# Kernel tuning notes

Measured on AMD Instinct MI355X. Metric: run time of the kernel, lower is better.

Reference implementation:

```python
import jax, jax.numpy as jnp
import numpy as np

B, L, P = 65536, 512, 96
E_LIN, E = 14, 16
FFT = 512
TEMP = 0.07
K = 2
EPS = 1e-5


def setup_inputs() -> dict:
    key = jax.random.key(0)
    k0, k1, k2 = jax.random.split(key, 3)
    x = jax.random.normal(k0, (B, L), dtype=jnp.float32)
    Wg = jax.random.normal(k1, (E, FFT // 2), dtype=jnp.float32) * 0.02
    bg = jnp.zeros((E,), dtype=jnp.float32)
    Wr = jax.random.normal(k2, (E_LIN, P, L), dtype=jnp.float32) * 0.02
    br = jnp.zeros((E_LIN, P), dtype=jnp.float32)
    return {"x": x, "Wg": Wg, "bg": bg, "Wr": Wr, "br": br}


def _periodogram(x):
    # x: [B, L] -> normalized power spectrum [B, FFT//2]
    x0 = x - jnp.mean(x, axis=1, keepdims=True)
    dft = jnp.fft.fft(x0, n=FFT, axis=1) / np.float32(np.sqrt(FFT))
    dft = dft[:, : FFT // 2]
    I = dft.real ** 2 + dft.imag ** 2
    s = jnp.sum(I, axis=1, keepdims=True)
    s = jnp.where(s == 0, jnp.ones_like(s), s)
    return I / s


def reference(x, Wg, bg, Wr, br):
    # gating (eval mode: no noise, divide by temperature)
    I = _periodogram(x)                                  # [B, F/2]
    gate = (I @ Wg.T + bg) / TEMP                        # [B, E]
    topv, topi = jax.lax.top_k(gate, K)                  # [B, K]
    gates = jax.nn.softmax(topv, axis=1)                 # [B, K]

    # RLinear experts: RevIN(norm) -> Linear -> RevIN(denorm); stats detached
    mu = jax.lax.stop_gradient(jnp.mean(x, axis=1, keepdims=True))        # [B,1]
    sd = jax.lax.stop_gradient(jnp.sqrt(jnp.var(x, axis=1, keepdims=True) + EPS))
    xn = (x - mu) / sd                                   # [B, L]
    yr = jnp.einsum('bl,epl->bep', xn, Wr) + br          # [B, E_LIN, P]
    yr = yr * sd[:, :, None] + mu[:, :, None]

    mean_out = jnp.broadcast_to(jnp.mean(x, axis=1, keepdims=True), (x.shape[0], P))[:, None, :]
    naive_out = jnp.broadcast_to(x[:, -1:], (x.shape[0], P))[:, None, :]

    eo = jnp.concatenate([yr, mean_out, naive_out], axis=1)   # [B, E, P]
    sel = jnp.take_along_axis(eo, topi[:, :, None], axis=1)   # [B, K, P]
    out = jnp.sum(gates[:, :, None] * sel, axis=1)            # [B, P]
    return out
```

## Files before the change

### kernel.cpp

```cpp
#include <hip/hip_runtime.h>
#include <math.h>

#define NB_B 65536
#define NL   512
#define NP   96
#define NE   16
#define NEL  14
#define NF   256
#define TEMP_INV (1.0f/0.07f)
#define TAU  1e-5f
#define PI_D 3.14159265358979323846
#define MAXCHK 1536

typedef __attribute__((ext_vector_type(8))) short bf16x8;
typedef __attribute__((ext_vector_type(4))) float f32x4;


#define WS_PCNT     0
#define WS_HOLES    16384
#define WS_PBASE    32768
#define WS_FLAGCNT  33792
#define WS_NCHK     33824
#define WS_HOLECNT  33840
#define WS_FLAG     33856
#define WS_SSUM     296000
#define WS_WGT      301376
#define WS_BGT      317760
#define WS_TWD      319872
#define WS_REC      328064
#define WS_HDR      590208
#define WS_RIDX     1638784
#define WS_WRB      1900928
#define WS_DESC     3473792
#define WS_XB16     3480064

__device__ __forceinline__ unsigned short f2bf(float f) {
    unsigned u = __float_as_uint(f);
    unsigned r = (u + 0x7fffu + ((u >> 16) & 1u)) >> 16;
    return (unsigned short)r;
}

__global__ __launch_bounds__(256) void k_prep(
    const float* __restrict__ Wg, const float* __restrict__ bg,
    const float* __restrict__ Wr,
    float* __restrict__ Ssum, float* __restrict__ WgE, float* __restrict__ bgT,
    double2* __restrict__ twd,
    int* __restrict__ pcnt, int* __restrict__ flagcnt, int* __restrict__ holecnt,
    ushort4* __restrict__ Wrb, int perm)
{
    int g = blockIdx.x * 256 + threadIdx.x;
    {
        ushort4 o = make_ushort4(0, 0, 0, 0);
        if (g < NEL * NP * NL / 4) {
            float4 v;
            if (perm) {
                int row = g >> 7, sq = g & 127;
                int ll = sq >> 1, kb = (sq & 1) * 4;
                const float* wr = Wr + (size_t)row * NL + ll;
                v.x = wr[(kb + 0) * 64]; v.y = wr[(kb + 1) * 64];
                v.z = wr[(kb + 2) * 64]; v.w = wr[(kb + 3) * 64];
            } else {
                v = ((const float4*)Wr)[g];
            }
            o.x = f2bf(v.x); o.y = f2bf(v.y); o.z = f2bf(v.z); o.w = f2bf(v.w);
        }
        Wrb[g] = o;
    }
    if (g < NEL * NP * 8) {
        int row = g >> 3, seg = g & 7;
        const float4* w = (const float4*)(Wr + (size_t)row * NL + seg * 64);
        float s = 0.f;
#pragma unroll
        for (int i = 0; i < 16; i++) { float4 v = w[i]; s += v.x + v.y + v.z + v.w; }
        s += __shfl_xor(s, 1); s += __shfl_xor(s, 2); s += __shfl_xor(s, 4);
        if (seg == 0) Ssum[row] = s;
    }
    if (g < 4096) {
        int c = g & 3, e = (g >> 2) & 15, f4 = g >> 6;
        WgE[g] = Wg[e * NF + f4 * 4 + c] * TEMP_INV;
    }
    if (g < 512) {
        double a = -2.0 * PI_D * (double)g / 512.0;
        twd[g] = make_double2(cos(a), sin(a));
    }
    if (g < 256) pcnt[g << 4] = 0;
    if (g < NE) bgT[g] = bg[g] * TEMP_INV;
    if (g == 300) *flagcnt = 0;
    if (g == 301) *holecnt = 0;
}

__global__ __launch_bounds__(256) void k_gate(
    const float* __restrict__ x,
    const float4* __restrict__ WgE4, const float* __restrict__ bgT,
    int* __restrict__ rec, float4* __restrict__ hdr,
    int* __restrict__ flaglist, int* __restrict__ flagcnt,
    int* __restrict__ pcnt, unsigned short* __restrict__ xb16)
{
    __shared__ __align__(16) float2 s_z[4][576];
    float* s_Iv = (float*)&s_z[0][0];

    const int t = threadIdx.x;
    const int wv = t >> 6, l = t & 63;
    const int b0 = blockIdx.x * 8 + wv * 2;

    const float th = -6.283185307179586f / 512.0f;
    const float R2 = 0.70710678118654752f;
    float s1, c1; __sincosf((float)l * th, &s1, &c1);
    float s2, c2; __sincosf((float)(2 * l) * th, &s2, &c2);
    float sw0, cw0; __sincosf((float)((l & 31) << 3) * th, &sw0, &cw0);
    float sw1, cw1; __sincosf((float)((l & 15) << 4) * th, &sw1, &cw1);
    float sw2, cw2; __sincosf((float)((l & 7) << 5) * th, &sw2, &cw2);
    float2 tw0[4];
    tw0[0] = make_float2(c1, s1);
    tw0[1] = make_float2(R2 * (c1 + s1), R2 * (s1 - c1));
    tw0[2] = make_float2(s1, -c1);
    tw0[3] = make_float2(tw0[1].y, -tw0[1].x);
    float2 tw1[2];
    tw1[0] = make_float2(c2, s2);
    tw1[1] = make_float2(s2, -c2);
    const float2 w2 = make_float2(c2 * c2 - s2 * s2, 2.f * c2 * s2);
    float2 wst[5];
    wst[0] = make_float2(cw0, sw0);
    wst[1] = make_float2(cw1, sw1);
    wst[2] = make_float2(cw2, sw2);
    {
        int j2 = l & 3;
        float cc3 = (j2 == 0) ? 1.f : (j2 == 1) ? R2 : (j2 == 2) ? 0.f : -R2;
        float ss3 = (j2 == 0) ? 0.f : (j2 == 2) ? -1.f : -R2;
        wst[3] = make_float2(cc3, ss3);
    }
    wst[4] = (l & 1) ? make_float2(0.f, -1.f) : make_float2(1.f, 0.f);

    const float* xa = x + (size_t)b0 * NL;
    const float* xb = xa + NL;
    float xr[8], xi[8];
#pragma unroll
    for (int k = 0; k < 8; k++) { xr[k] = xa[k * 64 + l]; xi[k] = xb[k * 64 + l]; }
    const float last_a = __shfl(xr[7], 63);
    const float last_b = __shfl(xi[7], 63);

    if (xb16) {
        unsigned pa_[4], pb_[4];
#pragma unroll
        for (int j = 0; j < 4; j++) {
            asm("v_cvt_pk_bf16_f32 %0, %1, %2" : "=v"(pa_[j]) : "v"(xr[2 * j]), "v"(xr[2 * j + 1]));
            asm("v_cvt_pk_bf16_f32 %0, %1, %2" : "=v"(pb_[j]) : "v"(xi[2 * j]), "v"(xi[2 * j + 1]));
        }
        *(uint4*)(xb16 + (size_t)b0 * NL + l * 8)       = *(uint4*)pa_;
        *(uint4*)(xb16 + (size_t)(b0 + 1) * NL + l * 8) = *(uint4*)pb_;
    }

#pragma unroll
    for (int k = 0; k < 4; k++) {
        float2 w = tw0[k];
        float ur = xr[k], ui = xi[k], vr = xr[k + 4], vi = xi[k + 4];
        xr[k] = ur + vr; xi[k] = ui + vi;
        float dr = ur - vr, di = ui - vi;
        xr[k + 4] = dr * w.x - di * w.y; xi[k + 4] = dr * w.y + di * w.x;
    }
    {
        const int kk[4] = {0, 1, 4, 5};
#pragma unroll
        for (int g2 = 0; g2 < 4; g2++) {
            int k = kk[g2];
            float2 w = tw1[k & 1];
            float ur = xr[k], ui = xi[k], vr = xr[k + 2], vi = xi[k + 2];
            xr[k] = ur + vr; xi[k] = ui + vi;
            float dr = ur - vr, di = ui - vi;
            xr[k + 2] = dr * w.x - di * w.y; xi[k + 2] = dr * w.y + di * w.x;
        }
    }
    {
#pragma unroll
        for (int k = 0; k < 8; k += 2) {
            float ur = xr[k], ui = xi[k], vr = xr[k + 1], vi = xi[k + 1];
            xr[k] = ur + vr; xi[k] = ui + vi;
            float dr = ur - vr, di = ui - vi;
            xr[k + 1] = dr * w2.x - di * w2.y; xi[k + 1] = dr * w2.y + di * w2.x;
        }
    }
#pragma unroll
    for (int st = 3; st < 8; st++) {
        const int half = 256 >> st;
        const float2 w = wst[st - 3];
        const bool up = (l & half) != 0;
        const float sg = up ? -1.f : 1.f;
        const float cc = up ? w.x : 1.f;
        const float ss = up ? w.y : 0.f;
#pragma unroll
        for (int k = 0; k < 8; k++) {
            float pr = __shfl_xor(xr[k], half);
            float pi = __shfl_xor(xi[k], half);
            float tr = fmaf(sg, xr[k], pr);
            float ti = fmaf(sg, xi[k], pi);
            xr[k] = tr * cc - ti * ss;
            xi[k] = tr * ss + ti * cc;
        }
    }
    {
        const float sg = (l & 1) ? -1.f : 1.f;
#pragma unroll
        for (int k = 0; k < 8; k++) {
            float pr = __shfl_xor(xr[k], 1);
            float pi = __shfl_xor(xi[k], 1);
            xr[k] = fmaf(sg, xr[k], pr);
            xi[k] = fmaf(sg, xi[k], pi);
        }
    }

#pragma unroll
    for (int k = 0; k < 8; k++) {
        int i = k * 64 + l;
        s_z[wv][i + (i >> 3)] = make_float2(xr[k], xi[k]);
    }

    float Ia[4], Ib[4];
    float psa = 0.f, psb = 0.f;
#pragma unroll
    for (int j = 0; j < 4; j++) {
        int f = (l << 2) | j;
        int i1_ = (int)(__brev((unsigned)f) >> 23);
        int i2_ = (int)(__brev((unsigned)((512 - f) & 511)) >> 23);
        float2 z1 = s_z[wv][i1_ + (i1_ >> 3)];
        float2 z2 = s_z[wv][i2_ + (i2_ >> 3)];
        float pr_ = z1.x + z2.x, qm = z1.y - z2.y;
        float qp = z1.y + z2.y, pm = z1.x - z2.x;
        float va = pr_ * pr_ + qm * qm;
        float vb = qp * qp + pm * pm;
        if (f == 0) { va = 0.f; vb = 0.f; }
        Ia[j] = va; Ib[j] = vb;
        psa += va; psb += vb;
    }
#pragma unroll
    for (int m = 1; m < 64; m <<= 1) {
        psa += __shfl_xor(psa, m); psb += __shfl_xor(psb, m);
    }
    const float psa_raw = psa, psb_raw = psb;
    if (psa == 0.f) psa = 1.f;
    if (psb == 0.f) psb = 1.f;
    const float inv_a = 1.f / psa, inv_b = 1.f / psb;

    const float2 Z0   = s_z[wv][0];
    const float2 Z256 = s_z[wv][1];

    float* wI = s_Iv + wv * 1152;
    const int io = (l << 2) + ((l >> 4) << 2);
    *(float4*)(wI + io)       = make_float4(Ia[0], Ia[1], Ia[2], Ia[3]);
    *(float4*)(wI + 272 + io) = make_float4(Ib[0], Ib[1], Ib[2], Ib[3]);

    const int e16 = l & 15, cq = l >> 4;
    const float bgv = bgT[e16];
    float accA = 0.f, accB = 0.f;
    const float* rA = wI + cq * 68;
    const float* rB = rA + 272;
#pragma unroll 4
    for (int jj = 0; jj < 16; jj++) {
        float4 ia = *(const float4*)(rA + 4 * jj);
        float4 ib = *(const float4*)(rB + 4 * jj);
        float4 w = WgE4[(cq * 16 + jj) * 16 + e16];
        accA += ia.x * w.x + ia.y * w.y + ia.z * w.z + ia.w * w.w;
        accB += ib.x * w.x + ib.y * w.y + ib.z * w.z + ib.w * w.w;
    }
    accA += __shfl_xor(accA, 16); accA += __shfl_xor(accA, 32);
    accB += __shfl_xor(accB, 16); accB += __shfl_xor(accB, 32);

    float v = ((l & 16) ? accB * inv_b : accA * inv_a) + bgv;

    float b0v = v; int b0i = e16;
#pragma unroll
    for (int m = 1; m < 16; m <<= 1) {
        float ov = __shfl_xor(b0v, m); int oi = __shfl_xor(b0i, m);
        if (ov > b0v || (ov == b0v && oi < b0i)) { b0v = ov; b0i = oi; }
    }
    float v1 = (e16 == b0i) ? -1e30f : v;
    float b1v = v1; int b1i = e16;
#pragma unroll
    for (int m = 1; m < 16; m <<= 1) {
        float ov = __shfl_xor(b1v, m); int oi = __shfl_xor(b1i, m);
        if (ov > b1v || (ov == b1v && oi < b1i)) { b1v = ov; b1i = oi; }
    }
    float v2 = (e16 == b1i) ? -1e30f : v1;
    float b2v = v2;
#pragma unroll
    for (int m = 1; m < 16; m <<= 1) {
        float ov = __shfl_xor(b2v, m);
        b2v = fmaxf(b2v, ov);
    }

    if (l == 0 || l == 16) {
        const int r = l >> 4;
        const int b = b0 + r;
        const float mu = (r ? Z0.y : Z0.x) * (1.f / 512.f);
        const float Jv = r ? Z256.y : Z256.x;
        const float ps = r ? psb_raw : psa_raw;
        const float sd = sqrtf((0.5f * ps + Jv * Jv) * (1.f / 262144.f) + 1e-5f);
        const float last = r ? last_b : last_a;
        const float w0 = 1.f / (1.f + expf(b1v - b0v));
        const int pid = b0i * 16 + b1i;
        const int lo = atomicAdd(&pcnt[pid << 4], 1);
        rec[b] = (pid << 24) | lo;
        hdr[b] = make_float4(mu, sd, last, w0);
        if (b1v - b2v < TAU) {
            int pos = atomicAdd(flagcnt, 1);
            flaglist[pos] = b;
        }
    }
}

__global__ __launch_bounds__(256) void k_refine(
    const float* __restrict__ x, const double2* __restrict__ twd,
    const float* __restrict__ Wg, const float* __restrict__ bg,
    int* __restrict__ rec, float4* __restrict__ hdr,
    const int* __restrict__ flaglist, const int* __restrict__ flagcnt,
    int* __restrict__ pcnt, int* __restrict__ holes, int* __restrict__ holecnt)
{
    __shared__ double s_x[512];
    __shared__ double s_I[256];
    __shared__ double s_red[16];
    __shared__ double s_g[16];
    const int nf = *flagcnt;
    const int t = threadIdx.x;
    const int wid = t >> 6, lane = t & 63;
    for (int fi = blockIdx.x; fi < nf; fi += gridDim.x) {
        const int b = flaglist[fi];
        const float* xp = x + (size_t)b * NL;
        double v0 = (double)xp[t], v1 = (double)xp[t + 256];
        double lsum = v0 + v1;
        for (int m = 1; m < 64; m <<= 1) lsum += __shfl_xor(lsum, m);
        if (lane == 0) s_red[wid] = lsum;
        __syncthreads();
        double mu = (s_red[0] + s_red[1] + s_red[2] + s_red[3]) * (1.0 / 512.0);
        s_x[t] = v0 - mu; s_x[t + 256] = v1 - mu;
        __syncthreads();
        double2 w = twd[t];
        double pr = 1.0, pi = 0.0, cr = 0.0, ci = 0.0;
        for (int n = 0; n < 512; n++) {
            double xv = s_x[n];
            cr += xv * pr; ci += xv * pi;
            double t2 = pr * w.x - pi * w.y;
            pi = pr * w.y + pi * w.x;
            pr = t2;
        }
        double I = cr * cr + ci * ci;
        s_I[t] = I;
        double ls = I;
        for (int m = 1; m < 64; m <<= 1) ls += __shfl_xor(ls, m);
        if (lane == 0) s_red[8 + wid] = ls;
        __syncthreads();
        double stot = s_red[8] + s_red[9] + s_red[10] + s_red[11];
        if (stot == 0.0) stot = 1.0;
        if (t < 16) {
            double acc = 0.0;
            const float* wrow = Wg + t * NF;
            for (int f = 0; f < NF; f++) acc += s_I[f] * (double)wrow[f];
            s_g[t] = (acc / stot + (double)bg[t]) * (1.0 / 0.07);
        }
        __syncthreads();
        if (t == 0) {
            double c0 = -1e300, c1 = -1e300; int j0 = 0, j1 = 0;
            for (int i = 0; i < 16; i++) {
                double v = s_g[i];
                if (v > c0) { c1 = c0; j1 = j0; c0 = v; j0 = i; }
                else if (v > c1) { c1 = v; j1 = i; }
            }
            double e1 = exp(c1 - c0);
            float w0f = (float)(1.0 / (1.0 + e1));
            int newpid = j0 * 16 + j1;
            int oldrec = rec[b];
            int oldpid = (int)(((unsigned)oldrec) >> 24);
            if (newpid == oldpid) {
                ((float*)(hdr + b))[3] = w0f;
            } else {
                int pos = atomicAdd(holecnt, 1);
                if (pos < 4096) {
                    int nlo = atomicAdd(&pcnt[newpid << 4], 1);
                    rec[b] = (newpid << 24) | nlo;
                    holes[pos] = oldrec;
                    ((float*)(hdr + b))[3] = w0f;
                }
            }
        }
        __syncthreads();
    }
}

__global__ __launch_bounds__(256) void k_scan(
    const int* __restrict__ pcnt, int* __restrict__ pbase,
    int* __restrict__ desc, int* __restrict__ nchk)
{
    __shared__ int s[256], c[256];
    const int t = threadIdx.x;
    const int n = pcnt[t << 4];
    s[t] = n;
    c[t] = (n + 63) >> 6;
    __syncthreads();
    for (int off = 1; off < 256; off <<= 1) {
        int v1 = (t >= off) ? s[t - off] : 0;
        int v2 = (t >= off) ? c[t - off] : 0;
        __syncthreads();
        s[t] += v1; c[t] += v2;
        __syncthreads();
    }
    int excl = t ? s[t - 1] : 0;
    int cexcl = t ? c[t - 1] : 0;
    pbase[t] = excl;
    int myc = (n + 63) >> 6;
    for (int j = 0; j < myc; j++) desc[cexcl + j] = (t << 16) | j;
    if (t == 255) *nchk = cexcl + myc;
}

__global__ __launch_bounds__(256) void k_scatter(
    const int* __restrict__ rec, const int* __restrict__ pbase,
    int* __restrict__ ridx,
    const int* __restrict__ holes, const int* __restrict__ holecnt)
{
    const int t = threadIdx.x;
    const int b = blockIdx.x * 256 + t;
    unsigned v = (unsigned)rec[b];
    ridx[pbase[v >> 24] + (v & 0xFFFFFF)] = b;
    if (blockIdx.x == 0) {
        int nh = *holecnt; if (nh > 4096) nh = 4096;
        for (int h = t; h < nh; h += 256) {
            unsigned hv = (unsigned)holes[h];
            ridx[pbase[hv >> 24] + (hv & 0xFFFFFF)] = -1;
        }
    }
}

template<int XB>
__global__ __launch_bounds__(256) void k_gemm(
    const float* __restrict__ x, const unsigned short* __restrict__ xb16,
    const unsigned short* __restrict__ Wrb,
    const float* __restrict__ br, const float* __restrict__ Ssum,
    const float4* __restrict__ hdr, float* __restrict__ out,
    const int* __restrict__ pcnt, const int* __restrict__ pbase,
    const int* __restrict__ ridx,
    const int* __restrict__ desc, const int* __restrict__ nchk)
{
    __shared__ __align__(16) unsigned short sA[64 * 72];
    __shared__ __align__(16) unsigned short sB[2][96 * 72];
    __shared__ int    s_idx[64];
    __shared__ float4 s_hdr[64];
    __shared__ float  s_br[2][96], s_S[2][96];
    if ((int)blockIdx.x >= *nchk) return;
    const int d = desc[blockIdx.x];
    const int pid = d >> 16, cc = d & 0xffff;
    const int n = pcnt[pid << 4];
    const int base = pbase[pid];
    const int i0 = pid >> 4, i1 = pid & 15;
    const int t = threadIdx.x;
    const int lane = t & 63, wv = t >> 6;
    const int quad = lane >> 4, l16 = lane & 15;
    const int ar = t >> 2, asub = t & 3;
    if (t < 96) {
        s_br[0][t] = (i0 < NEL) ? br[i0 * NP + t] : 0.f;
        s_S [0][t] = (i0 < NEL) ? Ssum[i0 * NP + t] : 0.f;
        s_br[1][t] = (i1 < NEL) ? br[i1 * NP + t] : 0.f;
        s_S [1][t] = (i1 < NEL) ? Ssum[i1 * NP + t] : 0.f;
    }
    if (t < 64) {
        int g = cc * 64 + t;
        bool vld = g < n;
        int row = vld ? ridx[base + g] : -1;
        s_idx[t] = row;
        s_hdr[t] = (row >= 0) ? hdr[row] : make_float4(0.f, 0.f, 0.f, 0.f);
    }
    __syncthreads();

    f32x4 acc[2][6];
#pragma unroll
    for (int ex = 0; ex < 2; ex++)
#pragma unroll
        for (int j = 0; j < 6; j++) acc[ex][j] = (f32x4){0.f, 0.f, 0.f, 0.f};

    int rr = s_idx[ar]; if (rr < 0) rr = 0;

    unsigned boff[6];
    unsigned short* bdst[6];
    const unsigned short* wb[2];
    wb[0] = Wrb + (size_t)i0 * NP * NL;
    wb[1] = Wrb + (size_t)i1 * NP * NL;
    int bex[6];
#pragma unroll
    for (int it = 0; it < 6; it++) {
        int ex = (it >= 3);
        int fl = t + (it - 3 * ex) * 256;
        int p = fl >> 3, kg = fl & 7;
        bex[it] = ex;
        boff[it] = (unsigned)(p * NL + kg * 8);
        bdst[it] = &sB[ex][p * 72 + kg * 8];
    }
    unsigned short* adst = sA + ar * 72 + asub * 16;

    const unsigned short* xrow16 = xb16 + (size_t)rr * NL + asub * 16;
    const float* xrowf = x + (size_t)rr * NL + asub * 16;

    bf16x8 aR[2]; float4 fA[4]; bf16x8 bR[6];

    if constexpr (XB) {
        aR[0] = *(const bf16x8*)(xrow16);
        aR[1] = *(const bf16x8*)(xrow16 + 8);
    } else {
#pragma unroll
        for (int i = 0; i < 4; i++) fA[i] = ((const float4*)xrowf)[i];
    }
#pragma unroll
    for (int it = 0; it < 6; it++) bR[it] = *(const bf16x8*)(wb[bex[it]] + boff[it]);

    for (int kb = 0; kb < NL; kb += 64) {
        if constexpr (XB) {
            *(bf16x8*)adst       = aR[0];
            *(bf16x8*)(adst + 8) = aR[1];
        } else {
            unsigned short tmp[16];
#pragma unroll
            for (int i = 0; i < 4; i++) {
                float4 v = fA[i];
                tmp[i * 4 + 0] = f2bf(v.x); tmp[i * 4 + 1] = f2bf(v.y);
                tmp[i * 4 + 2] = f2bf(v.z); tmp[i * 4 + 3] = f2bf(v.w);
            }
            *(bf16x8*)adst       = *(bf16x8*)tmp;
            *(bf16x8*)(adst + 8) = *(bf16x8*)(tmp + 8);
        }
#pragma unroll
        for (int it = 0; it < 6; it++) *(bf16x8*)bdst[it] = bR[it];
        __syncthreads();

        const int kn = kb + 64;
        if (kn < NL) {
            if constexpr (XB) {
                aR[0] = *(const bf16x8*)(xrow16 + kn);
                aR[1] = *(const bf16x8*)(xrow16 + kn + 8);
            } else {
#pragma unroll
                for (int i = 0; i < 4; i++) fA[i] = ((const float4*)(xrowf + kn))[i];
            }
#pragma unroll
            for (int it = 0; it < 6; it++)
                bR[it] = *(const bf16x8*)(wb[bex[it]] + boff[it] + kn);
        }

#pragma unroll
        for (int ks = 0; ks < 2; ks++) {
            bf16x8 af = *(const bf16x8*)(sA + (wv * 16 + l16) * 72 + ks * 32 + quad * 8);
#pragma unroll
            for (int ex = 0; ex < 2; ex++)
#pragma unroll
                for (int nt = 0; nt < 6; nt++) {
                    bf16x8 bf = *(const bf16x8*)(&sB[ex][(nt * 16 + l16) * 72 + ks * 32 + quad * 8]);
                    acc[ex][nt] = __builtin_amdgcn_mfma_f32_16x16x32_bf16(af, bf, acc[ex][nt], 0, 0, 0);
                }
        }
        __syncthreads();
    }
#pragma unroll
    for (int i = 0; i < 4; i++) {
        int rloc = wv * 16 + quad * 4 + i;
        int row = s_idx[rloc];
        if (row >= 0) {
            float4 h = s_hdr[rloc];
            float mu = h.x, sd = h.y, last = h.z, w0 = h.w, w1 = 1.f - w0;
            float* orow = out + (size_t)row * NP;
#pragma unroll
            for (int nt = 0; nt < 6; nt++) {
                int p = nt * 16 + l16;
                float v0 = (i0 < NEL) ? (mu + s_br[0][p] * sd - mu * s_S[0][p] + acc[0][nt][i])
                                      : (i0 == NEL ? mu : last);
                float v1 = (i1 < NEL) ? (mu + s_br[1][p] * sd - mu * s_S[1][p] + acc[1][nt][i])
                                      : (i1 == NEL ? mu : last);
                orow[p] = w0 * v0 + w1 * v1;
            }
        }
    }
}

extern "C" void kernel_launch(void* const* d_in, const int* in_sizes, int n_in,
                              void* d_out, int out_size, void* d_ws, size_t ws_size,
                              hipStream_t stream)
{
    const float* x  = (const float*)d_in[0];
    const float* Wg = (const float*)d_in[1];
    const float* bg = (const float*)d_in[2];
    const float* Wr = (const float*)d_in[3];
    const float* br = (const float*)d_in[4];
    float* out = (float*)d_out;
    char* ws = (char*)d_ws;

    int*     pcnt     = (int*)(ws + WS_PCNT);
    int*     holes    = (int*)(ws + WS_HOLES);
    int*     pbase    = (int*)(ws + WS_PBASE);
    int*     flagcnt  = (int*)(ws + WS_FLAGCNT);
    int*     nchk     = (int*)(ws + WS_NCHK);
    int*     holecnt  = (int*)(ws + WS_HOLECNT);
    int*     flaglist = (int*)(ws + WS_FLAG);
    float*   Ssum     = (float*)(ws + WS_SSUM);
    float*   WgE      = (float*)(ws + WS_WGT);
    float*   bgT      = (float*)(ws + WS_BGT);
    double2* twd      = (double2*)(ws + WS_TWD);
    int*     rec      = (int*)(ws + WS_REC);
    float4*  hdr      = (float4*)(ws + WS_HDR);
    int*     ridx     = (int*)(ws + WS_RIDX);
    unsigned short* Wrb = (unsigned short*)(ws + WS_WRB);
    int*     desc     = (int*)(ws + WS_DESC);

    const size_t xb_bytes = (size_t)NB_B * NL * 2;
    const int use_xb = (ws_size >= (size_t)WS_XB16 + xb_bytes);
    unsigned short* xb16 = use_xb ? (unsigned short*)(ws + WS_XB16) : (unsigned short*)0;

    k_prep<<<dim3(768), dim3(256), 0, stream>>>(Wg, bg, Wr, Ssum, WgE, bgT, twd,
                                                pcnt, flagcnt, holecnt,
                                                (ushort4*)Wrb, use_xb);
    k_gate<<<dim3(NB_B / 8), dim3(256), 0, stream>>>(x, (const float4*)WgE, bgT,
                                                     rec, hdr, flaglist, flagcnt, pcnt, xb16);
    k_refine<<<dim3(512), dim3(256), 0, stream>>>(x, twd, Wg, bg, rec, hdr,
                                                  flaglist, flagcnt, pcnt, holes, holecnt);
    k_scan<<<dim3(1), dim3(256), 0, stream>>>(pcnt, pbase, desc, nchk);
    k_scatter<<<dim3(NB_B / 256), dim3(256), 0, stream>>>(rec, pbase, ridx, holes, holecnt);
    if (use_xb)
        k_gemm<1><<<dim3(MAXCHK), dim3(256), 0, stream>>>(x, xb16, Wrb, br, Ssum, hdr, out,
                                                          pcnt, pbase, ridx, desc, nchk);
    else
        k_gemm<0><<<dim3(MAXCHK), dim3(256), 0, stream>>>(x, xb16, Wrb, br, Ssum, hdr, out,
                                                          pcnt, pbase, ridx, desc, nchk);
}
```

Baseline: 296.7 us.

## Add register-direct MFMA GEMM with pre-swizzled bf16 expert weight fragments

Adds a second bf16 copy of the expert weights, pre-arranged in k_prep into the exact MFMA B-fragment order so each lane loads its operand with one contiguous 16-byte read. A new GEMM kernel reads A fragments from the bf16 copy of x and B fragments straight from global memory into registers, dropping the shared-memory staging and barriers of the old tiled kernel. Each block computes both selected experts for 64 rows and applies the RevIN denorm and gate blend in the epilogue. The cost is heavy register use, about 24 bf16x8 B fragments in flight per k-step, and repeated weight reads served from cache instead of LDS. The new path also needs a larger workspace and falls back to the old kernel when the workspace is too small.

```diff
diff --git a/kernel.cpp b/kernel.cpp
--- a/kernel.cpp
+++ b/kernel.cpp
@@ -33,6 +33,8 @@
 #define WS_WRB      1900928
 #define WS_DESC     3473792
 #define WS_XB16     3480064
+#define WS_WRBF     70588928
+#define WS_WRBF_END 72161792
 
 __device__ __forceinline__ unsigned short f2bf(float f) {
     unsigned u = __float_as_uint(f);
@@ -46,7 +48,7 @@
     float* __restrict__ Ssum, float* __restrict__ WgE, float* __restrict__ bgT,
     double2* __restrict__ twd,
     int* __restrict__ pcnt, int* __restrict__ flagcnt, int* __restrict__ holecnt,
-    ushort4* __restrict__ Wrb, int perm)
+    ushort4* __restrict__ Wrb, ushort4* __restrict__ WrbF, int perm)
 {
     int g = blockIdx.x * 256 + threadIdx.x;
     {
@@ -65,6 +67,33 @@
             o.x = f2bf(v.x); o.y = f2bf(v.y); o.z = f2bf(v.z); o.w = f2bf(v.w);
         }
         Wrb[g] = o;
+    }
+    if (WrbF) {
+        ushort4 o = make_ushort4(0, 0, 0, 0);
+        int idx  = g >> 1;
+        int lane = idx & 63;
+        int idx2 = idx >> 6;
+        int nt   = idx2 % 6;
+        int idx3 = idx2 / 6;
+        int ks   = idx3 & 1;
+        int idx4 = idx3 >> 1;
+        int kb8  = idx4 & 7;
+        int e    = idx4 >> 3;
+        if (e < NEL) {
+            int p = nt * 16 + (lane & 15);
+            int quad = lane >> 4;
+            int skb = kb8 * 64 + ks * 32 + quad * 8 + (g & 1) * 4;
+            const float* wr = Wr + ((size_t)e * NP + p) * NL;
+            float vv[4];
+#pragma unroll
+            for (int jj = 0; jj < 4; jj++) {
+                int sk = skb + jj;
+                int ko = perm ? ((sk & 7) * 64 + (sk >> 3)) : sk;
+                vv[jj] = wr[ko];
+            }
+            o.x = f2bf(vv[0]); o.y = f2bf(vv[1]); o.z = f2bf(vv[2]); o.w = f2bf(vv[3]);
+        }
+        WrbF[g] = o;
     }
     if (g < NEL * NP * 8) {
         int row = g >> 3, seg = g & 7;
@@ -423,6 +452,97 @@
         for (int h = t; h < nh; h += 256) {
             unsigned hv = (unsigned)holes[h];
             ridx[pbase[hv >> 24] + (hv & 0xFFFFFF)] = -1;
+        }
+    }
+}
+
+__global__ __launch_bounds__(256) void k_gemm_reg(
+    const unsigned short* __restrict__ xb16,
+    const unsigned short* __restrict__ WrbF,
+    const float* __restrict__ br, const float* __restrict__ Ssum,
+    const float4* __restrict__ hdr, float* __restrict__ out,
+    const int* __restrict__ pcnt, const int* __restrict__ pbase,
+    const int* __restrict__ ridx,
+    const int* __restrict__ desc, const int* __restrict__ nchk)
+{
+    __shared__ int    s_idx[64];
+    __shared__ float4 s_hdr[64];
+    __shared__ float  s_br[2][96], s_S[2][96];
+    if ((int)blockIdx.x >= *nchk) return;
+    const int d = desc[blockIdx.x];
+    const int pid = d >> 16, cc = d & 0xffff;
+    const int n = pcnt[pid << 4];
+    const int base = pbase[pid];
+    const int i0 = pid >> 4, i1 = pid & 15;
+    const int t = threadIdx.x;
+    const int lane = t & 63, wv = t >> 6;
+    const int quad = lane >> 4, l16 = lane & 15;
+    if (t < 96) {
+        s_br[0][t] = (i0 < NEL) ? br[i0 * NP + t] : 0.f;
+        s_S [0][t] = (i0 < NEL) ? Ssum[i0 * NP + t] : 0.f;
+        s_br[1][t] = (i1 < NEL) ? br[i1 * NP + t] : 0.f;
+        s_S [1][t] = (i1 < NEL) ? Ssum[i1 * NP + t] : 0.f;
+    }
+    if (t < 64) {
+        int g = cc * 64 + t;
+        bool vld = g < n;
+        int row = vld ? ridx[base + g] : -1;
+        s_idx[t] = row;
+        s_hdr[t] = (row >= 0) ? hdr[row] : make_float4(0.f, 0.f, 0.f, 0.f);
+    }
+    __syncthreads();
+
+    int myrow = s_idx[wv * 16 + l16]; if (myrow < 0) myrow = 0;
+    const unsigned short* aP = xb16 + (size_t)myrow * NL + quad * 8;
+    const unsigned short* bP[2];
+    bP[0] = WrbF + (size_t)i0 * 49152 + lane * 8;
+    bP[1] = WrbF + (size_t)i1 * 49152 + lane * 8;
+
+    f32x4 acc[2][6];
+#pragma unroll
+    for (int ex = 0; ex < 2; ex++)
+#pragma unroll
+        for (int j = 0; j < 6; j++) acc[ex][j] = (f32x4){0.f, 0.f, 0.f, 0.f};
+
+#pragma unroll
+    for (int kb8 = 0; kb8 < 8; kb8++) {
+        bf16x8 a0 = *(const bf16x8*)(aP + kb8 * 64);
+        bf16x8 a1 = *(const bf16x8*)(aP + kb8 * 64 + 32);
+        bf16x8 bfr[2][2][6];
+#pragma unroll
+        for (int ks = 0; ks < 2; ks++)
+#pragma unroll
+            for (int ex = 0; ex < 2; ex++)
+#pragma unroll
+                for (int nt = 0; nt < 6; nt++)
+                    bfr[ks][ex][nt] = *(const bf16x8*)(bP[ex] + kb8 * 6144 + ks * 3072 + nt * 512);
+#pragma unroll
+        for (int ks = 0; ks < 2; ks++)
+#pragma unroll
+            for (int ex = 0; ex < 2; ex++)
+#pragma unroll
+                for (int nt = 0; nt < 6; nt++)
+                    acc[ex][nt] = __builtin_amdgcn_mfma_f32_16x16x32_bf16(
+                        ks ? a1 : a0, bfr[ks][ex][nt], acc[ex][nt], 0, 0, 0);
+    }
+
+#pragma unroll
+    for (int i = 0; i < 4; i++) {
+        int rloc = wv * 16 + quad * 4 + i;
+        int row = s_idx[rloc];
+        if (row >= 0) {
+            float4 h = s_hdr[rloc];
+            float mu = h.x, sd = h.y, last = h.z, w0 = h.w, w1 = 1.f - w0;
+            float* orow = out + (size_t)row * NP;
+#pragma unroll
+            for (int nt = 0; nt < 6; nt++) {
+                int p = nt * 16 + l16;
+                float v0 = (i0 < NEL) ? (mu + s_br[0][p] * sd - mu * s_S[0][p] + acc[0][nt][i])
+                                      : (i0 == NEL ? mu : last);
+                float v1 = (i1 < NEL) ? (mu + s_br[1][p] * sd - mu * s_S[1][p] + acc[1][nt][i])
+                                      : (i1 == NEL ? mu : last);
+                orow[p] = w0 * v0 + w1 * v1;
+            }
         }
     }
 }
@@ -603,20 +723,24 @@
     unsigned short* Wrb = (unsigned short*)(ws + WS_WRB);
     int*     desc     = (int*)(ws + WS_DESC);
 
-    const size_t xb_bytes = (size_t)NB_B * NL * 2;
-    const int use_xb = (ws_size >= (size_t)WS_XB16 + xb_bytes);
-    unsigned short* xb16 = use_xb ? (unsigned short*)(ws + WS_XB16) : (unsigned short*)0;
+    const int use_xb  = (ws_size >= (size_t)WS_WRBF);
+    const int use_xb2 = (ws_size >= (size_t)WS_WRBF_END);
+    unsigned short* xb16 = use_xb  ? (unsigned short*)(ws + WS_XB16) : (unsigned short*)0;
+    unsigned short* WrbF = use_xb2 ? (unsigned short*)(ws + WS_WRBF) : (unsigned short*)0;
 
     k_prep<<<dim3(768), dim3(256), 0, stream>>>(Wg, bg, Wr, Ssum, WgE, bgT, twd,
                                                 pcnt, flagcnt, holecnt,
-                                                (ushort4*)Wrb, use_xb);
+                                                (ushort4*)Wrb, (ushort4*)WrbF, use_xb);
     k_gate<<<dim3(NB_B / 8), dim3(256), 0, stream>>>(x, (const float4*)WgE, bgT,
                                                      rec, hdr, flaglist, flagcnt, pcnt, xb16);
     k_refine<<<dim3(512), dim3(256), 0, stream>>>(x, twd, Wg, bg, rec, hdr,
                                                   flaglist, flagcnt, pcnt, holes, holecnt);
     k_scan<<<dim3(1), dim3(256), 0, stream>>>(pcnt, pbase, desc, nchk);
     k_scatter<<<dim3(NB_B / 256), dim3(256), 0, stream>>>(rec, pbase, ridx, holes, holecnt);
-    if (use_xb)
+    if (use_xb2)
+        k_gemm_reg<<<dim3(MAXCHK), dim3(256), 0, stream>>>(xb16, WrbF, br, Ssum, hdr, out,
+                                                           pcnt, pbase, ridx, desc, nchk);
+    else if (use_xb)
         k_gemm<1><<<dim3(MAXCHK), dim3(256), 0, stream>>>(x, xb16, Wrb, br, Ssum, hdr, out,
                                                           pcnt, pbase, ridx, desc, nchk);
     else
```

Measured after the change: 311.9 us. 1.05x slower.
